# Performance work log

Hardware: AMD Instinct MI355X
Metric: run time of the kernel (lower is better)

The kernel has to match this reference:

```python
import jax, jax.numpy as jnp
import numpy as np

# Irreps structure: (multiplicity, component dim 2l+1) for 64x0e + 32x1o + 16x2e
MULTS = (64, 32, 16)
DIMS = (1, 3, 5)
N_NODES = 65536
NUM_TYPES = 64


def setup_inputs() -> dict:
    key = jax.random.key(0)
    k_x, k_idx, k0, k1, k2 = jax.random.split(key, 5)
    dim = sum(m * d for m, d in zip(MULTS, DIMS))  # 240
    x = jax.random.normal(k_x, (N_NODES, dim), dtype=jnp.float32)
    idx = jax.random.randint(k_idx, (N_NODES,), 0, NUM_TYPES)
    W0 = jax.random.normal(k0, (NUM_TYPES, 64, 64), dtype=jnp.float32)
    W1 = jax.random.normal(k1, (NUM_TYPES, 32, 32), dtype=jnp.float32)
    W2 = jax.random.normal(k2, (NUM_TYPES, 16, 16), dtype=jnp.float32)
    return {"x": x, "W0": W0, "W1": W1, "W2": W2, "idx": idx}


def reference(x, W0, W1, W2, idx):
    """Indexed e3nn-style linear: per-node index gathers a weight set; each
    irrep block mixes multiplicity channels (shared across the 2l+1 components)
    with e3nn path normalization 1/sqrt(m_in)."""
    n = x.shape[0]
    outs = []
    off = 0
    for W, m, d in zip((W0, W1, W2), MULTS, DIMS):
        blk = x[:, off:off + m * d].reshape(n, m, d)  # [N, m_in, 2l+1]
        off += m * d
        Wn = W[idx]  # gather per-node weights: [N, m_in, m_out]
        scale = np.float32(1.0 / np.sqrt(m))
        out = jnp.einsum('nio,nid->nod', Wn, blk) * scale  # [N, m_out, 2l+1]
        outs.append(out.reshape(n, m * d))
    return jnp.concatenate(outs, axis=-1)
```

## Files before the change

kernel.cpp:

```cpp
#include <hip/hip_runtime.h>

typedef __attribute__((ext_vector_type(8))) short short8;
typedef __attribute__((ext_vector_type(4))) float floatx4;

#define NTYPES    64
#define WT_STRIDE 5632
#define ROWS_PB   64
#define THREADS   256
#define ROW_U     248
#define CPAD      16

__device__ __forceinline__ unsigned short f2bf(float f) {
    union { float f; unsigned u; } v; v.f = f;
    unsigned u = v.u;
    u += 0x7FFFu + ((u >> 16) & 1u);
    return (unsigned short)(u >> 16);
}

__global__ __launch_bounds__(256) void wt_kernel(const float* __restrict__ W0,
                                                 const float* __restrict__ W1,
                                                 const float* __restrict__ W2,
                                                 unsigned short* __restrict__ wt,
                                                 int* __restrict__ gcount) {
    __shared__ float ws0[4096];
    __shared__ float ws1[1024];
    __shared__ float ws2[256];
    const int t = blockIdx.x, tid = threadIdx.x;
    if (t == 0 && tid < NTYPES) gcount[tid * CPAD] = 0;
    const float4* s0 = (const float4*)(W0 + (size_t)t * 4096);
#pragma unroll
    for (int j = 0; j < 4; ++j) ((float4*)ws0)[j * 256 + tid] = s0[j * 256 + tid];
    ((float4*)ws1)[tid] = ((const float4*)(W1 + (size_t)t * 1024))[tid];
    if (tid < 64) ((float4*)ws2)[tid] = ((const float4*)(W2 + (size_t)t * 256))[tid];
    __syncthreads();
    unsigned short* dst = wt + (size_t)t * WT_STRIDE;
    for (int e = tid; e < 4096; e += 256) {
        int f = e >> 9, rem = e & 511, rr = rem >> 5, k2 = rem & 31;
        int i = (f & 1) * 32 + k2, o = (f >> 1) * 16 + rr;
        dst[e] = f2bf(ws0[i * 64 + o] * 0.125f);
    }
    for (int e = tid; e < 1024; e += 256) {
        int h = e >> 9, rem = e & 511, rr = rem >> 5, k = rem & 31;
        dst[4096 + e] = f2bf(ws1[k * 32 + h * 16 + rr] * 0.17677669529663687f);
    }
    for (int e = tid; e < 512; e += 256) {
        int rr = e >> 5, k = e & 31;
        dst[5120 + e] = (k < 16) ? f2bf(ws2[k * 16 + rr] * 0.25f) : (unsigned short)0;
    }
}

__global__ __launch_bounds__(256) void hist_kernel(const int* __restrict__ idx,
                                                   int* __restrict__ gcount, int n) {
    __shared__ int c[NTYPES];
    const int tid = threadIdx.x, g = blockIdx.x * 256 + tid;
    if (tid < NTYPES) c[tid] = 0;
    __syncthreads();
    if (g < n) atomicAdd(&c[idx[g]], 1);
    __syncthreads();
    if (tid < NTYPES && c[tid]) atomicAdd(&gcount[tid * CPAD], c[tid]);
}

__global__ __launch_bounds__(64) void base_kernel(const int* __restrict__ gcount,
                                                  int* __restrict__ gcur) {
    const int t = threadIdx.x;
    int v = gcount[t * CPAD];
    int s = v;
#pragma unroll
    for (int o = 1; o < 64; o <<= 1) {
        int u = __shfl_up(s, o);
        if (t >= o) s += u;
    }
    gcur[t * CPAD] = s - v;
}

__global__ __launch_bounds__(256) void scatter_kernel(const int* __restrict__ idx,
                                                      int* __restrict__ gcur,
                                                      int* __restrict__ psort, int n) {
    __shared__ int c[NTYPES], off[NTYPES], cur[NTYPES];
    const int tid = threadIdx.x, g = blockIdx.x * 256 + tid;
    if (tid < NTYPES) { c[tid] = 0; cur[tid] = 0; }
    __syncthreads();
    int ty = -1;
    if (g < n) { ty = idx[g]; atomicAdd(&c[ty], 1); }
    __syncthreads();
    if (tid < NTYPES && c[tid]) off[tid] = atomicAdd(&gcur[tid * CPAD], c[tid]);
    __syncthreads();
    if (g < n) {
        int rk = atomicAdd(&cur[ty], 1);
        psort[off[ty] + rk] = g | (ty << 24);
    }
}

__global__ __launch_bounds__(THREADS, 4) void main_kernel(
    const float* __restrict__ x,
    const int* __restrict__ psort,
    const unsigned short* __restrict__ wt,
    float* __restrict__ out, int n)
{
    __shared__ __align__(16) unsigned short xrow[ROWS_PB * ROW_U];
    __shared__ int pls[ROWS_PB];
    __shared__ int tinfo[ROWS_PB];
    __shared__ int ntiles;

    const int b = blockIdx.x, tid = threadIdx.x;
    const int nbase = b * ROWS_PB;
    const int nv = min(ROWS_PB, n - nbase);
    const int wv = tid >> 6, ln = tid & 63;

    if (tid < ROWS_PB) pls[tid] = (nbase + tid < n) ? psort[nbase + tid] : 0;
    __syncthreads();

    if (wv == 0) {
        int v = (ln < nv) ? (pls[ln] >> 24) : -1;
        int pv = __shfl_up(v, 1);
        bool bnd = (ln < nv) && (ln == 0 || v != pv);
        unsigned long long bm = __ballot(bnd);
        if (ln == 0) {
            int ntl = 0;
            unsigned long long m = bm;
            while (m) {
                unsigned long long m2 = m & (m - 1);
                int s = (int)__builtin_ctzll(m);
                int e = m2 ? (int)__builtin_ctzll(m2) : nv;
                int t = pls[s] >> 24;
                for (int q = s; q < e; q += 16)
                    tinfo[ntl++] = (t << 16) | (q << 8) | min(16, e - q);
                m = m2;
            }
            ntiles = ntl;
        }
    }

#pragma unroll
    for (int it = 0; it < 15; ++it) {
        int e = it * THREADS + tid;
        int row = e / 60, c4 = e - row * 60;
        if (row < nv) {
            int node = pls[row] & 0xFFFFFF;
            float4 f = *(const float4*)(x + (size_t)node * 240 + c4 * 4);
            unsigned short qq[4] = {f2bf(f.x), f2bf(f.y), f2bf(f.z), f2bf(f.w)};
            unsigned short* xr = xrow + row * ROW_U;
            if (c4 < 16) {
                *(ushort4*)(xr + c4 * 4) = ushort4{qq[0], qq[1], qq[2], qq[3]};
            } else if (c4 < 40) {
                int t0 = c4 * 4 - 64;
                int i = t0 / 3, d = t0 - i * 3;
#pragma unroll
                for (int j = 0; j < 4; ++j) {
                    xr[64 + d * 32 + i] = qq[j];
                    if (++d == 3) { d = 0; ++i; }
                }
            } else {
                int t0 = c4 * 4 - 160;
                int i = t0 / 5, d = t0 - i * 5;
#pragma unroll
                for (int j = 0; j < 4; ++j) {
                    xr[160 + d * 16 + i] = qq[j];
                    if (++d == 5) { d = 0; ++i; }
                }
            }
        }
    }
    __syncthreads();

    const int r = ln & 15, q4 = ln >> 4;
    const int NT = ntiles;

    for (int ti = wv; ti < NT; ti += (THREADS / 64)) {
        const int info = tinfo[ti];
        const int ty = info >> 16, s0 = (info >> 8) & 0xFF, rows = info & 0xFF;
        const int lrow = s0 + min(r, rows - 1);
        const unsigned short* xr = xrow + lrow * ROW_U;
        const unsigned short* wb = wt + (size_t)ty * WT_STRIDE;
        const bool vst = (r < rows);
        const int gnode = vst ? (pls[s0 + r] & 0xFFFFFF) : 0;
        float* op = out + (size_t)gnode * 240;

        short8 bx0 = *(const short8*)(xr + q4 * 8);
        short8 bx1 = *(const short8*)(xr + 32 + q4 * 8);

#pragma unroll
        for (int nt = 0; nt < 4; ++nt) {
            short8 wa = *(const short8*)(wb + (nt * 2) * 512 + r * 32 + q4 * 8);
            short8 wc = *(const short8*)(wb + (nt * 2 + 1) * 512 + r * 32 + q4 * 8);
            floatx4 ac = {0.f, 0.f, 0.f, 0.f};
            ac = __builtin_amdgcn_mfma_f32_16x16x32_bf16(wa, bx0, ac, 0, 0, 0);
            ac = __builtin_amdgcn_mfma_f32_16x16x32_bf16(wc, bx1, ac, 0, 0, 0);
            if (vst) *(floatx4*)(op + nt * 16 + q4 * 4) = ac;
        }

        {
            short8 wc0 = *(const short8*)(wb + 4096 + r * 32 + q4 * 8);
            short8 wc1 = *(const short8*)(wb + 4096 + 512 + r * 32 + q4 * 8);
            floatx4 a1[2][3];
#pragma unroll
            for (int d = 0; d < 3; ++d) {
                short8 bx = *(const short8*)(xr + 64 + d * 32 + q4 * 8);
                floatx4 z = {0.f, 0.f, 0.f, 0.f};
                a1[0][d] = __builtin_amdgcn_mfma_f32_16x16x32_bf16(wc0, bx, z, 0, 0, 0);
                a1[1][d] = __builtin_amdgcn_mfma_f32_16x16x32_bf16(wc1, bx, z, 0, 0, 0);
            }
            if (vst) {
#pragma unroll
                for (int h = 0; h < 2; ++h) {
                    float* o1 = op + 64 + (h * 16 + q4 * 4) * 3;
                    floatx4 v0 = {a1[h][0][0], a1[h][1][0], a1[h][2][0], a1[h][0][1]};
                    floatx4 v1 = {a1[h][1][1], a1[h][2][1], a1[h][0][2], a1[h][1][2]};
                    floatx4 v2 = {a1[h][2][2], a1[h][0][3], a1[h][1][3], a1[h][2][3]};
                    *(floatx4*)(o1)     = v0;
                    *(floatx4*)(o1 + 4) = v1;
                    *(floatx4*)(o1 + 8) = v2;
                }
            }
        }

        {
            short8 wc2 = *(const short8*)(wb + 5120 + r * 32 + q4 * 8);
            floatx4 a2[5];
#pragma unroll
            for (int d = 0; d < 5; ++d) {
                short8 bx = *(const short8*)(xr + 160 + d * 16 + (q4 & 1) * 8);
                floatx4 z = {0.f, 0.f, 0.f, 0.f};
                a2[d] = __builtin_amdgcn_mfma_f32_16x16x32_bf16(wc2, bx, z, 0, 0, 0);
            }
            if (vst) {
                float* o2 = op + 160 + q4 * 20;
                floatx4 v0 = {a2[0][0], a2[1][0], a2[2][0], a2[3][0]};
                floatx4 v1 = {a2[4][0], a2[0][1], a2[1][1], a2[2][1]};
                floatx4 v2 = {a2[3][1], a2[4][1], a2[0][2], a2[1][2]};
                floatx4 v3 = {a2[2][2], a2[3][2], a2[4][2], a2[0][3]};
                floatx4 v4 = {a2[1][3], a2[2][3], a2[3][3], a2[4][3]};
                *(floatx4*)(o2)      = v0;
                *(floatx4*)(o2 + 4)  = v1;
                *(floatx4*)(o2 + 8)  = v2;
                *(floatx4*)(o2 + 12) = v3;
                *(floatx4*)(o2 + 16) = v4;
            }
        }
    }
}

extern "C" void kernel_launch(void* const* d_in, const int* in_sizes, int n_in,
                              void* d_out, int out_size, void* d_ws, size_t ws_size,
                              hipStream_t stream) {
    const float* x  = (const float*)d_in[0];
    const float* W0 = (const float*)d_in[1];
    const float* W1 = (const float*)d_in[2];
    const float* W2 = (const float*)d_in[3];
    const int*   idx = (const int*)d_in[4];
    float* out = (float*)d_out;
    const int n = in_sizes[4];
    const int nb = (n + 255) / 256;

    char* ws = (char*)d_ws;
    unsigned short* wt = (unsigned short*)ws;
    size_t off = (size_t)NTYPES * WT_STRIDE * 2;
    int* psort  = (int*)(ws + off); off += (size_t)n * 4;
    int* gcount = (int*)(ws + off); off += (size_t)NTYPES * CPAD * 4;
    int* gcur   = (int*)(ws + off);

    wt_kernel     <<<NTYPES, 256, 0, stream>>>(W0, W1, W2, wt, gcount);
    hist_kernel   <<<nb, 256, 0, stream>>>(idx, gcount, n);
    base_kernel   <<<1, 64, 0, stream>>>(gcount, gcur);
    scatter_kernel<<<nb, 256, 0, stream>>>(idx, gcur, psort, n);
    main_kernel   <<<(n + ROWS_PB - 1) / ROWS_PB, THREADS, 0, stream>>>(x, psort, wt, out, n);
}
```

Measured before the change: 148.8 us.

## Use single-wave 16-row blocks with in-register segment handling per type

Main kernel now launches one 64-thread wave per 16 sorted rows instead of four waves per 64 rows. Tile metadata in shared memory is replaced by shuffles and a ballot over type boundaries. Each type segment reuses B operands hoisted into registers and masks stores to its rows. This removes block-wide syncs and the serial tile-list build and raises the block count. In exchange, a 16-row window that straddles type boundaries runs the full MFMA set once per segment, and more blocks means more launch and scheduling overhead.

```diff
diff --git a/kernel.cpp b/kernel.cpp
--- a/kernel.cpp
+++ b/kernel.cpp
@@ -5,8 +5,7 @@
 
 #define NTYPES    64
 #define WT_STRIDE 5632
-#define ROWS_PB   64
-#define THREADS   256
+#define WROWS     16
 #define ROW_U     248
 #define CPAD      16
 
@@ -91,52 +90,28 @@
     }
 }
 
-__global__ __launch_bounds__(THREADS, 4) void main_kernel(
+__global__ __launch_bounds__(64, 4) void main_kernel(
     const float* __restrict__ x,
     const int* __restrict__ psort,
     const unsigned short* __restrict__ wt,
     float* __restrict__ out, int n)
 {
-    __shared__ __align__(16) unsigned short xrow[ROWS_PB * ROW_U];
-    __shared__ int pls[ROWS_PB];
-    __shared__ int tinfo[ROWS_PB];
-    __shared__ int ntiles;
-
-    const int b = blockIdx.x, tid = threadIdx.x;
-    const int nbase = b * ROWS_PB;
-    const int nv = min(ROWS_PB, n - nbase);
-    const int wv = tid >> 6, ln = tid & 63;
-
-    if (tid < ROWS_PB) pls[tid] = (nbase + tid < n) ? psort[nbase + tid] : 0;
-    __syncthreads();
-
-    if (wv == 0) {
-        int v = (ln < nv) ? (pls[ln] >> 24) : -1;
-        int pv = __shfl_up(v, 1);
-        bool bnd = (ln < nv) && (ln == 0 || v != pv);
-        unsigned long long bm = __ballot(bnd);
-        if (ln == 0) {
-            int ntl = 0;
-            unsigned long long m = bm;
-            while (m) {
-                unsigned long long m2 = m & (m - 1);
-                int s = (int)__builtin_ctzll(m);
-                int e = m2 ? (int)__builtin_ctzll(m2) : nv;
-                int t = pls[s] >> 24;
-                for (int q = s; q < e; q += 16)
-                    tinfo[ntl++] = (t << 16) | (q << 8) | min(16, e - q);
-                m = m2;
-            }
-            ntiles = ntl;
-        }
-    }
+    __shared__ __align__(16) unsigned short xrow[WROWS * ROW_U];
+
+    const int b = blockIdx.x, ln = threadIdx.x;
+    const int nbase = b * WROWS;
+    const int nv = min(WROWS, n - nbase);
+
+    int pl = 0;
+    if (ln < WROWS && (nbase + ln) < n) pl = psort[nbase + ln];
 
 #pragma unroll
     for (int it = 0; it < 15; ++it) {
-        int e = it * THREADS + tid;
+        int e = it * 64 + ln;
         int row = e / 60, c4 = e - row * 60;
+        int prow = __shfl(pl, row);
         if (row < nv) {
-            int node = pls[row] & 0xFFFFFF;
+            int node = prow & 0xFFFFFF;
             float4 f = *(const float4*)(x + (size_t)node * 240 + c4 * 4);
             unsigned short qq[4] = {f2bf(f.x), f2bf(f.y), f2bf(f.z), f2bf(f.w)};
             unsigned short* xr = xrow + row * ROW_U;
@@ -164,20 +139,33 @@
     __syncthreads();
 
     const int r = ln & 15, q4 = ln >> 4;
-    const int NT = ntiles;
-
-    for (int ti = wv; ti < NT; ti += (THREADS / 64)) {
-        const int info = tinfo[ti];
-        const int ty = info >> 16, s0 = (info >> 8) & 0xFF, rows = info & 0xFF;
-        const int lrow = s0 + min(r, rows - 1);
-        const unsigned short* xr = xrow + lrow * ROW_U;
-        const unsigned short* wb = wt + (size_t)ty * WT_STRIDE;
-        const bool vst = (r < rows);
-        const int gnode = vst ? (pls[s0 + r] & 0xFFFFFF) : 0;
-        float* op = out + (size_t)gnode * 240;
-
-        short8 bx0 = *(const short8*)(xr + q4 * 8);
-        short8 bx1 = *(const short8*)(xr + 32 + q4 * 8);
+
+    const unsigned short* xr = xrow + min(r, nv - 1) * ROW_U;
+    short8 bx0 = *(const short8*)(xr + q4 * 8);
+    short8 bx1 = *(const short8*)(xr + 32 + q4 * 8);
+    short8 b1d[3];
+#pragma unroll
+    for (int d = 0; d < 3; ++d) b1d[d] = *(const short8*)(xr + 64 + d * 32 + q4 * 8);
+    short8 b2d[5];
+#pragma unroll
+    for (int d = 0; d < 5; ++d) b2d[d] = *(const short8*)(xr + 160 + d * 16 + (q4 & 1) * 8);
+
+    const int prow_r = __shfl(pl, r);
+    const bool vrow = (r < nv);
+    float* op = out + (size_t)(prow_r & 0xFFFFFF) * 240;
+
+    int ti  = __shfl(pl, r) >> 24;
+    int tim = __shfl(pl, (r > 0) ? (r - 1) : 0) >> 24;
+    bool bnd = (r == 0) || (ti != tim);
+    unsigned m = (unsigned)(__ballot(bnd) & 0xFFFFull);
+
+    while (m) {
+        const int slo = __builtin_ctz(m);
+        const unsigned m2 = m & (m - 1u);
+        const int shi = m2 ? __builtin_ctz(m2) : nv;
+        const int tyseg = __shfl(pl, slo) >> 24;
+        const unsigned short* wb = wt + (size_t)tyseg * WT_STRIDE;
+        const bool vst = vrow && (r >= slo) && (r < shi);
 
 #pragma unroll
         for (int nt = 0; nt < 4; ++nt) {
@@ -195,10 +183,9 @@
             floatx4 a1[2][3];
 #pragma unroll
             for (int d = 0; d < 3; ++d) {
-                short8 bx = *(const short8*)(xr + 64 + d * 32 + q4 * 8);
                 floatx4 z = {0.f, 0.f, 0.f, 0.f};
-                a1[0][d] = __builtin_amdgcn_mfma_f32_16x16x32_bf16(wc0, bx, z, 0, 0, 0);
-                a1[1][d] = __builtin_amdgcn_mfma_f32_16x16x32_bf16(wc1, bx, z, 0, 0, 0);
+                a1[0][d] = __builtin_amdgcn_mfma_f32_16x16x32_bf16(wc0, b1d[d], z, 0, 0, 0);
+                a1[1][d] = __builtin_amdgcn_mfma_f32_16x16x32_bf16(wc1, b1d[d], z, 0, 0, 0);
             }
             if (vst) {
 #pragma unroll
@@ -219,9 +206,8 @@
             floatx4 a2[5];
 #pragma unroll
             for (int d = 0; d < 5; ++d) {
-                short8 bx = *(const short8*)(xr + 160 + d * 16 + (q4 & 1) * 8);
                 floatx4 z = {0.f, 0.f, 0.f, 0.f};
-                a2[d] = __builtin_amdgcn_mfma_f32_16x16x32_bf16(wc2, bx, z, 0, 0, 0);
+                a2[d] = __builtin_amdgcn_mfma_f32_16x16x32_bf16(wc2, b2d[d], z, 0, 0, 0);
             }
             if (vst) {
                 float* o2 = op + 160 + q4 * 20;
@@ -237,6 +223,7 @@
                 *(floatx4*)(o2 + 16) = v4;
             }
         }
+        m = m2;
     }
 }
 
@@ -263,5 +250,5 @@
     hist_kernel   <<<nb, 256, 0, stream>>>(idx, gcount, n);
     base_kernel   <<<1, 64, 0, stream>>>(gcount, gcur);
     scatter_kernel<<<nb, 256, 0, stream>>>(idx, gcur, psort, n);
-    main_kernel   <<<(n + ROWS_PB - 1) / ROWS_PB, THREADS, 0, stream>>>(x, psort, wt, out, n);
-}
+    main_kernel   <<<(n + WROWS - 1) / WROWS, 64, 0, stream>>>(x, psort, wt, out, n);
+}
```

Measured after the change: 150.0 us. About the same (+0.8%).
